# Kernel tuning notes

Measured on AMD Instinct MI355X. Metric: run time of the kernel, lower is better.

Reference implementation:

```python
import jax, jax.numpy as jnp
import numpy as np

# Static config mirroring FinalFFTAudioEngine(compression_ratio=0.3)
COMPRESSION_RATIO = 0.3
ENERGY_THRESHOLD = 0.05
WINDOW = 256  # window_size=512 -> power-of-2 loop ends at 512 -> min(512//2, 512) = 256


def _important_mask(energy, min_count, threshold):
    """Threshold mask, replaced by top-k mask if too few survive (faithful to torch code)."""
    th_mask = energy > threshold
    _, idx = jax.lax.top_k(energy, min_count)
    tk_mask = jnp.zeros(energy.shape, dtype=bool).at[idx].set(True)
    return jnp.where(jnp.sum(th_mask) < min_count, tk_mask, th_mask)


def setup_inputs() -> dict:
    key = jax.random.key(0)
    weight_matrix = jax.random.normal(key, (4096, 4096), dtype=jnp.float32)
    return {"weight_matrix": weight_matrix}


def reference(weight_matrix):
    # weight_to_audio_signal: flatten + max-abs normalize
    signal = weight_matrix.reshape(-1).astype(jnp.float32)
    n = signal.shape[0]  # 16777216, exact multiple of WINDOW -> no padding branch
    sig_max = jnp.max(jnp.abs(signal))
    norm = jnp.where(sig_max > 1e-10, sig_max, jnp.float32(1.0))
    signal = signal / norm

    # optimized_spectral_analysis: non-overlapping windows + per-window FFT
    windows = signal.reshape(-1, WINDOW)          # [T, F] = [65536, 256]
    spec = jnp.fft.fft(windows)                   # complex64 [T, F]

    # intelligent_frequency_selection
    energy = jnp.abs(spec) ** 2                   # [T, F]
    freq_energy = jnp.mean(energy, axis=0)        # [F]
    time_energy = jnp.mean(energy, axis=1)        # [T]
    min_freqs = max(1, int(WINDOW * (1.0 - COMPRESSION_RATIO * 0.7)))          # 202
    min_times = max(1, int(windows.shape[0] * (1.0 - COMPRESSION_RATIO * 0.7)))  # 51773
    freq_mask = _important_mask(freq_energy, min_freqs,
                                ENERGY_THRESHOLD * jnp.max(freq_energy))
    time_mask = _important_mask(time_energy, min_times,
                                ENERGY_THRESHOLD * jnp.max(time_energy))

    # lossless_compression: fused masked copy (replaces nested python double-for-loop)
    mask2d = time_mask[:, None] & freq_mask[None, :]
    compressed = jnp.where(mask2d, spec, jnp.zeros((), dtype=spec.dtype))

    # perfect_reconstruction: IFFT, take real part, flatten, trim to original length
    recon = jnp.real(jnp.fft.ifft(compressed)).reshape(-1)[:n]
    return recon
```

## Files before the change

kernel.cpp:

```cpp
#include <hip/hip_runtime.h>

#define N_TOTAL   16777216
#define NWIN      65536
#define MIN_FREQS 202
#define MIN_TIMES 51773
#define NSLOTS    64
#define NBLK      1024

#define IDX_TCNT    2
#define IDX_FMALL   3
#define IDX_TTHR    4
#define IDX_INVNORM 5
#define IDX_FCNT    6
#define IDX_FMASK   8
#define IDX_SLOTS   264
#define IDX_AMAXB   16648
#define IDX_TMAXB   18696
#define IDX_SUMSQ   20744
#define IDX_TMASKA  86280

__device__ __forceinline__ float dpp_row_sum16(float x)
{
    x += __int_as_float(__builtin_amdgcn_mov_dpp(__float_as_int(x), 0xB1,  0xF, 0xF, true));
    x += __int_as_float(__builtin_amdgcn_mov_dpp(__float_as_int(x), 0x4E,  0xF, 0xF, true));
    x += __int_as_float(__builtin_amdgcn_mov_dpp(__float_as_int(x), 0x141, 0xF, 0xF, true));
    x += __int_as_float(__builtin_amdgcn_mov_dpp(__float_as_int(x), 0x140, 0xF, 0xF, true));
    return x;
}

__device__ __forceinline__ void fft16(float ar[16], float ai[16])
{
#define SWP(a,b) { float t_=ar[a]; ar[a]=ar[b]; ar[b]=t_; \
                   t_=ai[a]; ai[a]=ai[b]; ai[b]=t_; }
    SWP(1,8) SWP(2,4) SWP(3,12) SWP(5,10) SWP(7,14) SWP(11,13)
#undef SWP
#pragma unroll
    for (int i = 0; i < 16; i += 2) {
        float tr = ar[i+1], ti = ai[i+1];
        ar[i+1] = ar[i] - tr; ai[i+1] = ai[i] - ti;
        ar[i] += tr;          ai[i] += ti;
    }
#pragma unroll
    for (int i = 0; i < 16; i += 4) {
        { float tr = ar[i+2], ti = ai[i+2];
          ar[i+2] = ar[i] - tr; ai[i+2] = ai[i] - ti; ar[i] += tr; ai[i] += ti; }
        { float tr = ai[i+3], ti = -ar[i+3];
          ar[i+3] = ar[i+1] - tr; ai[i+3] = ai[i+1] - ti; ar[i+1] += tr; ai[i+1] += ti; }
    }
#pragma unroll
    for (int i = 0; i < 16; i += 8) {
        { float tr = ar[i+4], ti = ai[i+4];
          ar[i+4] = ar[i] - tr; ai[i+4] = ai[i] - ti; ar[i] += tr; ai[i] += ti; }
        { float br = ar[i+5], bi = ai[i+5];
          float tr = 0.70710678f * (br + bi), ti = 0.70710678f * (bi - br);
          ar[i+5] = ar[i+1] - tr; ai[i+5] = ai[i+1] - ti; ar[i+1] += tr; ai[i+1] += ti; }
        { float tr = ai[i+6], ti = -ar[i+6];
          ar[i+6] = ar[i+2] - tr; ai[i+6] = ai[i+2] - ti; ar[i+2] += tr; ai[i+2] += ti; }
        { float br = ar[i+7], bi = ai[i+7];
          float tr = 0.70710678f * (bi - br), ti = -0.70710678f * (br + bi);
          ar[i+7] = ar[i+3] - tr; ai[i+7] = ai[i+3] - ti; ar[i+3] += tr; ai[i+3] += ti; }
    }
    { float tr = ar[8], ti = ai[8];
      ar[8] = ar[0] - tr; ai[8] = ai[0] - ti; ar[0] += tr; ai[0] += ti; }
#define BUT(J, WR, WI) { float br = ar[8+J], bi = ai[8+J];     \
      float tr = br*(WR) - bi*(WI), ti = br*(WI) + bi*(WR);    \
      ar[8+J] = ar[J] - tr; ai[8+J] = ai[J] - ti; ar[J] += tr; ai[J] += ti; }
    BUT(1,  0.92387953f, -0.38268343f)
    BUT(2,  0.70710678f, -0.70710678f)
    BUT(3,  0.38268343f, -0.92387953f)
    BUT(4,  0.f, -1.f)
    BUT(5, -0.38268343f, -0.92387953f)
    BUT(6, -0.70710678f, -0.70710678f)
    BUT(7, -0.92387953f, -0.38268343f)
#undef BUT
}

__global__ __launch_bounds__(256) void k_stats(const float* __restrict__ x,
                                               float* __restrict__ W)
{
    __shared__ float B[16][552];
    __shared__ float sE[256];
    __shared__ float red[256];
    const int tid  = threadIdx.x;
    const int lane = tid & 63;
    const int wv   = tid >> 6;
    const int subw = lane >> 4;
    const int n2   = lane & 15;
    float* Bs = B[wv * 4 + subw];
    float2* Bs2 = (float2*)Bs;

    float twr[16], twi[16];
    {
        float cs, sn;
        __sincosf(-0.024543692606170f * (float)n2, &sn, &cs);
        twr[0] = 1.f; twi[0] = 0.f;
#pragma unroll
        for (int k = 1; k < 16; ++k) {
            twr[k] = twr[k-1] * cs - twi[k-1] * sn;
            twi[k] = twr[k-1] * sn + twi[k-1] * cs;
        }
    }

    float e[16];
#pragma unroll
    for (int k = 0; k < 16; ++k) e[k] = 0.f;
    float amax = 0.f, tmx = 0.f;
    float* sumsq = W + IDX_SUMSQ;

    const int wave_gid = (blockIdx.x << 2) | wv;
    const int GSTRIDE  = 4 * NBLK;

    const float4* xg = (const float4*)(x + (size_t)wave_gid * 1024);
    float4 v0 = xg[lane];
    float4 v1 = xg[64 + lane];
    float4 v2 = xg[128 + lane];
    float4 v3 = xg[192 + lane];

#pragma unroll 1
    for (int g = wave_gid; g < NWIN / 4; g += GSTRIDE) {
        *(float4*)&B[wv * 4 + 0][lane * 4] = v0;
        *(float4*)&B[wv * 4 + 1][lane * 4] = v1;
        *(float4*)&B[wv * 4 + 2][lane * 4] = v2;
        *(float4*)&B[wv * 4 + 3][lane * 4] = v3;
        amax = fmaxf(amax, fmaxf(fmaxf(fabsf(v0.x), fabsf(v0.y)),
                                 fmaxf(fabsf(v0.z), fabsf(v0.w))));
        amax = fmaxf(amax, fmaxf(fmaxf(fabsf(v1.x), fabsf(v1.y)),
                                 fmaxf(fabsf(v1.z), fabsf(v1.w))));
        amax = fmaxf(amax, fmaxf(fmaxf(fabsf(v2.x), fabsf(v2.y)),
                                 fmaxf(fabsf(v2.z), fabsf(v2.w))));
        amax = fmaxf(amax, fmaxf(fmaxf(fabsf(v3.x), fabsf(v3.y)),
                                 fmaxf(fabsf(v3.z), fabsf(v3.w))));
        const int gn = g + GSTRIDE;
        if (gn < NWIN / 4) {
            const float4* xn = (const float4*)(x + (size_t)gn * 1024);
            v0 = xn[lane];
            v1 = xn[64 + lane];
            v2 = xn[128 + lane];
            v3 = xn[192 + lane];
        }
        asm volatile("s_waitcnt lgkmcnt(0)" ::: "memory");
        __builtin_amdgcn_sched_barrier(0);
        float ar[16], ai[16];
#pragma unroll
        for (int j = 0; j < 16; ++j) { ar[j] = Bs[16 * j + n2]; ai[j] = 0.f; }

        fft16(ar, ai);

#pragma unroll
        for (int k = 1; k < 16; ++k) {
            const float xr = ar[k], xi = ai[k];
            ar[k] = xr * twr[k] - xi * twi[k];
            ai[k] = xr * twi[k] + xi * twr[k];
        }

#pragma unroll
        for (int k = 0; k < 16; ++k)
            Bs2[17 * k + n2] = make_float2(ar[k], ai[k]);
        asm volatile("s_waitcnt lgkmcnt(0)" ::: "memory");
        __builtin_amdgcn_sched_barrier(0);
#pragma unroll
        for (int k = 0; k < 16; ++k) {
            const float2 t = Bs2[17 * n2 + k];
            ar[k] = t.x; ai[k] = t.y;
        }

        fft16(ar, ai);

        float p = 0.f;
#pragma unroll
        for (int k = 0; k < 16; ++k) {
            const float t = fmaf(ar[k], ar[k], ai[k] * ai[k]);
            e[k] += t; p += t;
        }
        p = dpp_row_sum16(p);
        if (n2 == 0) sumsq[g * 4 + subw] = p;
        tmx = fmaxf(tmx, p);
    }

    sE[tid] = 0.f;
    __syncthreads();
#pragma unroll
    for (int k = 0; k < 16; ++k)
        atomicAdd(&sE[k * 16 + n2], e[k]);
    __syncthreads();
    atomicAdd(&W[IDX_SLOTS + (size_t)(blockIdx.x & (NSLOTS - 1)) * 256 + tid], sE[tid]);

    red[tid] = amax; __syncthreads();
    for (int s = 128; s > 0; s >>= 1) {
        if (tid < s) red[tid] = fmaxf(red[tid], red[tid + s]);
        __syncthreads();
    }
    if (tid == 0) W[IDX_AMAXB + blockIdx.x] = red[0];
    __syncthreads();
    red[tid] = tmx; __syncthreads();
    for (int s = 128; s > 0; s >>= 1) {
        if (tid < s) red[tid] = fmaxf(red[tid], red[tid + s]);
        __syncthreads();
    }
    if (tid == 0) W[IDX_TMAXB + blockIdx.x] = red[0];
}

__global__ __launch_bounds__(256) void k_post(float* __restrict__ W)
{
    __shared__ float red[256];
    const int tid = threadIdx.x;

    if (blockIdx.x != 0) {
        float tm = 0.f;
#pragma unroll
        for (int k = 0; k < NBLK / 256; ++k)
            tm = fmaxf(tm, W[IDX_TMAXB + k * 256 + tid]);
        red[tid] = tm; __syncthreads();
        for (int s = 128; s > 0; s >>= 1) {
            if (tid < s) red[tid] = fmaxf(red[tid], red[tid + s]);
            __syncthreads();
        }
        const float tthr = 0.05f * red[0];
        __syncthreads();
        const float* sumsq = W + IDX_SUMSQ;
        float* tmask = W + IDX_TMASKA;
        const int base = (blockIdx.x - 1) * 1024 + tid;
        int c = 0;
#pragma unroll
        for (int k = 0; k < 4; k++) {
            const int i = base + k * 256;
            const int mm = (sumsq[i] > tthr) ? 1 : 0;
            c += mm;
            tmask[i] = (float)mm;
        }
        red[tid] = (float)c; __syncthreads();
        for (int s = 128; s > 0; s >>= 1) {
            if (tid < s) red[tid] += red[tid + s];
            __syncthreads();
        }
        if (tid == 0) atomicAdd((int*)W + IDX_TCNT, (int)red[0]);
        return;
    }

    __shared__ float e[256];
    float am = 0.f;
#pragma unroll
    for (int k = 0; k < NBLK / 256; ++k)
        am = fmaxf(am, W[IDX_AMAXB + k * 256 + tid]);
    red[tid] = am; __syncthreads();
    for (int s = 128; s > 0; s >>= 1) {
        if (tid < s) red[tid] = fmaxf(red[tid], red[tid + s]);
        __syncthreads();
    }
    const float amax = red[0];
    __syncthreads();

    float acc = 0.f;
#pragma unroll
    for (int s = 0; s < NSLOTS; s++) acc += W[IDX_SLOTS + s * 256 + tid];
    e[tid] = acc;
    red[tid] = acc; __syncthreads();
    for (int s = 128; s > 0; s >>= 1) {
        if (tid < s) red[tid] = fmaxf(red[tid], red[tid + s]);
        __syncthreads();
    }
    const float fthr = 0.05f * red[0];
    __syncthreads();
    const int my = (acc > fthr) ? 1 : 0;
    red[tid] = (float)my; __syncthreads();
    for (int s = 128; s > 0; s >>= 1) {
        if (tid < s) red[tid] += red[tid + s];
        __syncthreads();
    }
    const int fcnt = (int)red[0];
    __syncthreads();
    float m;
    if (fcnt >= MIN_FREQS) {
        m = (float)my;
    } else {
        int rank = 0;
        for (int j = 0; j < 256; j++) {
            const float ej = e[j];
            if (ej > acc || (ej == acc && j < tid)) rank++;
        }
        m = (rank < MIN_FREQS) ? 1.f : 0.f;
    }
    W[IDX_FMASK + tid] = m;
    red[tid] = m; __syncthreads();
    for (int s = 128; s > 0; s >>= 1) {
        if (tid < s) red[tid] += red[tid + s];
        __syncthreads();
    }
    if (tid == 0) {
        ((int*)W)[IDX_FMALL] = ((int)red[0] == 256) ? 1 : 0;
        ((int*)W)[IDX_FCNT]  = fcnt;
        W[IDX_INVNORM] = 1.f / ((amax > 1e-10f) ? amax : 1.f);
    }
}

__global__ __launch_bounds__(256) void k_timefb(float* __restrict__ W)
{
    if (((const int*)W)[IDX_TCNT] >= MIN_TIMES) return;
    const int t = blockIdx.x * 256 + threadIdx.x;
    const float* sumsq = W + IDX_SUMSQ;
    const float st = sumsq[t];
    int rank = 0;
    for (int j = 0; j < NWIN; j++) {
        const float sj = sumsq[j];
        if (sj > st || (sj == st && j < t)) rank++;
    }
    W[IDX_TMASKA + t] = (rank < MIN_TIMES) ? 1.f : 0.f;
}

__global__ __launch_bounds__(256) void k_out(const float* __restrict__ x,
                                             float* __restrict__ out,
                                             const float* __restrict__ W)
{
    const int tid = threadIdx.x;
    const int fm_all = ((const int*)W)[IDX_FMALL];
    const float inv_norm = W[IDX_INVNORM];
    if (fm_all) {
        const float4* xi = (const float4*)x;
        float4* yo = (float4*)out;
        const float* tmask = W + IDX_TMASKA;
        for (int i = blockIdx.x * 256 + tid; i < N_TOTAL / 4; i += gridDim.x * 256) {
            const float s = inv_norm * tmask[i >> 6];
            float4 v = xi[i];
            v.x *= s; v.y *= s; v.z *= s; v.w *= s;
            yo[i] = v;
        }
        return;
    }
    __shared__ float re[256], im[256], twr[128], twi[128], fm[256];
    if (tid < 128) {
        float s, c;
        __sincosf(-6.283185307179586f * (float)tid / 256.0f, &s, &c);
        twr[tid] = c; twi[tid] = s;
    }
    fm[tid] = W[IDX_FMASK + (int)(__brev((unsigned)tid) >> 24)];
    __syncthreads();
    const float scale = inv_norm * (1.f / 256.f);
    for (int w = blockIdx.x; w < NWIN; w += gridDim.x) {
        const float tm = W[IDX_TMASKA + w];
        if (tm == 0.f) { out[w * 256 + tid] = 0.f; continue; }
        re[tid] = x[w * 256 + tid]; im[tid] = 0.f;
        __syncthreads();
        for (int lh = 7; lh >= 0; lh--) {
            const int half = 1 << lh;
            if (tid < 128) {
                const int k  = tid & (half - 1);
                const int i0 = ((tid & ~(half - 1)) << 1) | k;
                const int i1 = i0 + half;
                const float ar = re[i0], ai = im[i0], br = re[i1], bi = im[i1];
                const float dr = ar - br, di = ai - bi;
                re[i0] = ar + br; im[i0] = ai + bi;
                const int ti = k << (7 - lh);
                const float wr = twr[ti], wi = twi[ti];
                re[i1] = dr * wr - di * wi;
                im[i1] = dr * wi + di * wr;
            }
            __syncthreads();
        }
        re[tid] *= fm[tid]; im[tid] *= fm[tid];
        __syncthreads();
        for (int lh = 0; lh < 8; lh++) {
            const int half = 1 << lh;
            if (tid < 128) {
                const int k  = tid & (half - 1);
                const int i0 = ((tid & ~(half - 1)) << 1) | k;
                const int i1 = i0 + half;
                const int ti = k << (7 - lh);
                const float wr = twr[ti], wi = -twi[ti];
                const float br = re[i1], bi = im[i1];
                const float tr = br * wr - bi * wi;
                const float ts = br * wi + bi * wr;
                const float ar = re[i0], ai = im[i0];
                re[i1] = ar - tr; im[i1] = ai - ts;
                re[i0] = ar + tr; im[i0] = ai + ts;
            }
            __syncthreads();
        }
        out[w * 256 + tid] = re[tid] * scale;
        __syncthreads();
    }
}

extern "C" void kernel_launch(void* const* d_in, const int* in_sizes, int n_in,
                              void* d_out, int out_size, void* d_ws, size_t ws_size,
                              hipStream_t stream)
{
    const float* x = (const float*)d_in[0];
    float* out = (float*)d_out;
    float* W = (float*)d_ws;
    hipMemsetAsync(d_ws, 0, (size_t)IDX_AMAXB * sizeof(float), stream);
    hipLaunchKernelGGL(k_stats,  dim3(NBLK), dim3(256), 0, stream, x, W);
    hipLaunchKernelGGL(k_post,   dim3(65),   dim3(256), 0, stream, W);
    hipLaunchKernelGGL(k_timefb, dim3(256),  dim3(256), 0, stream, W);
    hipLaunchKernelGGL(k_out,    dim3(2048), dim3(256), 0, stream, x, out, W);
}
```

Before: 83.35 us.

## Shrink LDS transpose buffer and recompute twiddles to raise occupancy in stats kernel

The k_stats kernel's per-subwave shared buffer is halved by transposing the real and imaginary parts in two separate passes instead of as interleaved float2. Twiddle factors are now recomputed on the fly by recurrence rather than held in 32 registers, and the grid block count is doubled. The aim is lower LDS and VGPR pressure so more waves fit per CU, plus better spread across CUs. The cost is an extra LDS round-trip and wait per window and a few extra multiplies per twiddle, and the recurrence runs each iteration.

```diff
diff --git a/kernel.cpp b/kernel.cpp
--- a/kernel.cpp
+++ b/kernel.cpp
@@ -5,7 +5,7 @@
 #define MIN_FREQS 202
 #define MIN_TIMES 51773
 #define NSLOTS    64
-#define NBLK      1024
+#define NBLK      2048
 
 #define IDX_TCNT    2
 #define IDX_FMALL   3
@@ -78,7 +78,7 @@
 __global__ __launch_bounds__(256) void k_stats(const float* __restrict__ x,
                                                float* __restrict__ W)
 {
-    __shared__ float B[16][552];
+    __shared__ float B[16][272];
     __shared__ float sE[256];
     __shared__ float red[256];
     const int tid  = threadIdx.x;
@@ -87,19 +87,9 @@
     const int subw = lane >> 4;
     const int n2   = lane & 15;
     float* Bs = B[wv * 4 + subw];
-    float2* Bs2 = (float2*)Bs;
-
-    float twr[16], twi[16];
-    {
-        float cs, sn;
-        __sincosf(-0.024543692606170f * (float)n2, &sn, &cs);
-        twr[0] = 1.f; twi[0] = 0.f;
-#pragma unroll
-        for (int k = 1; k < 16; ++k) {
-            twr[k] = twr[k-1] * cs - twi[k-1] * sn;
-            twi[k] = twr[k-1] * sn + twi[k-1] * cs;
-        }
-    }
+
+    float cs, sn;
+    __sincosf(-0.024543692606170f * (float)n2, &sn, &cs);
 
     float e[16];
 #pragma unroll
@@ -146,23 +136,30 @@
 
         fft16(ar, ai);
 
-#pragma unroll
-        for (int k = 1; k < 16; ++k) {
-            const float xr = ar[k], xi = ai[k];
-            ar[k] = xr * twr[k] - xi * twi[k];
-            ai[k] = xr * twi[k] + xi * twr[k];
-        }
-
-#pragma unroll
-        for (int k = 0; k < 16; ++k)
-            Bs2[17 * k + n2] = make_float2(ar[k], ai[k]);
+        { float wr = 1.f, wi = 0.f;
+#pragma unroll
+          for (int k = 1; k < 16; ++k) {
+              const float nwr = wr * cs - wi * sn;
+              const float nwi = wr * sn + wi * cs;
+              wr = nwr; wi = nwi;
+              const float xr = ar[k], xi = ai[k];
+              ar[k] = xr * wr - xi * wi;
+              ai[k] = xr * wi + xi * wr;
+          } }
+
+#pragma unroll
+        for (int k = 0; k < 16; ++k) Bs[17 * k + n2] = ar[k];
         asm volatile("s_waitcnt lgkmcnt(0)" ::: "memory");
         __builtin_amdgcn_sched_barrier(0);
 #pragma unroll
-        for (int k = 0; k < 16; ++k) {
-            const float2 t = Bs2[17 * n2 + k];
-            ar[k] = t.x; ai[k] = t.y;
-        }
+        for (int k = 0; k < 16; ++k) ar[k] = Bs[17 * n2 + k];
+        asm volatile("" ::: "memory");
+#pragma unroll
+        for (int k = 0; k < 16; ++k) Bs[17 * k + n2] = ai[k];
+        asm volatile("s_waitcnt lgkmcnt(0)" ::: "memory");
+        __builtin_amdgcn_sched_barrier(0);
+#pragma unroll
+        for (int k = 0; k < 16; ++k) ai[k] = Bs[17 * n2 + k];
 
         fft16(ar, ai);
 
```

After: 103.2 us. +23.8%, slower.

## Compute per-window spectral energy with bf16 MFMA DFT instead of radix-16 FFT

Applied to the files above, without the earlier changes.

The statistics kernel drops its two-pass radix-16 FFT and instead multiplies bf16-converted windows by a bf16 DFT matrix held in registers, using 32x32x16 MFMA instructions, to get per-frequency energy. Per-window time energy now comes directly from the time-domain sum of squares (Parseval) rather than from the spectrum. Blocks grow to 1024 threads, each block handles 256 windows with a double-buffered LDS stage, and the grid shrinks from 1024 to 256 blocks. This aims to cut VALU and LDS shuffle work in the stats pass. In exchange, rounding inputs and twiddles to bf16 can flip frequency-mask decisions that sit near the threshold.

```diff
diff --git a/kernel.cpp b/kernel.cpp
--- a/kernel.cpp
+++ b/kernel.cpp
@@ -5,7 +5,7 @@
 #define MIN_FREQS 202
 #define MIN_TIMES 51773
 #define NSLOTS    64
-#define NBLK      1024
+#define NBLK      256
 
 #define IDX_TCNT    2
 #define IDX_FMALL   3
@@ -19,6 +19,9 @@
 #define IDX_SUMSQ   20744
 #define IDX_TMASKA  86280
 
+typedef __attribute__((ext_vector_type(8)))  short bf16x8;
+typedef __attribute__((ext_vector_type(16))) float f32x16;
+
 __device__ __forceinline__ float dpp_row_sum16(float x)
 {
     x += __int_as_float(__builtin_amdgcn_mov_dpp(__float_as_int(x), 0xB1,  0xF, 0xF, true));
@@ -28,176 +31,121 @@
     return x;
 }
 
-__device__ __forceinline__ void fft16(float ar[16], float ai[16])
-{
-#define SWP(a,b) { float t_=ar[a]; ar[a]=ar[b]; ar[b]=t_; \
-                   t_=ai[a]; ai[a]=ai[b]; ai[b]=t_; }
-    SWP(1,8) SWP(2,4) SWP(3,12) SWP(5,10) SWP(7,14) SWP(11,13)
-#undef SWP
-#pragma unroll
-    for (int i = 0; i < 16; i += 2) {
-        float tr = ar[i+1], ti = ai[i+1];
-        ar[i+1] = ar[i] - tr; ai[i+1] = ai[i] - ti;
-        ar[i] += tr;          ai[i] += ti;
-    }
-#pragma unroll
-    for (int i = 0; i < 16; i += 4) {
-        { float tr = ar[i+2], ti = ai[i+2];
-          ar[i+2] = ar[i] - tr; ai[i+2] = ai[i] - ti; ar[i] += tr; ai[i] += ti; }
-        { float tr = ai[i+3], ti = -ar[i+3];
-          ar[i+3] = ar[i+1] - tr; ai[i+3] = ai[i+1] - ti; ar[i+1] += tr; ai[i+1] += ti; }
-    }
-#pragma unroll
-    for (int i = 0; i < 16; i += 8) {
-        { float tr = ar[i+4], ti = ai[i+4];
-          ar[i+4] = ar[i] - tr; ai[i+4] = ai[i] - ti; ar[i] += tr; ai[i] += ti; }
-        { float br = ar[i+5], bi = ai[i+5];
-          float tr = 0.70710678f * (br + bi), ti = 0.70710678f * (bi - br);
-          ar[i+5] = ar[i+1] - tr; ai[i+5] = ai[i+1] - ti; ar[i+1] += tr; ai[i+1] += ti; }
-        { float tr = ai[i+6], ti = -ar[i+6];
-          ar[i+6] = ar[i+2] - tr; ai[i+6] = ai[i+2] - ti; ar[i+2] += tr; ai[i+2] += ti; }
-        { float br = ar[i+7], bi = ai[i+7];
-          float tr = 0.70710678f * (bi - br), ti = -0.70710678f * (br + bi);
-          ar[i+7] = ar[i+3] - tr; ai[i+7] = ai[i+3] - ti; ar[i+3] += tr; ai[i+3] += ti; }
-    }
-    { float tr = ar[8], ti = ai[8];
-      ar[8] = ar[0] - tr; ai[8] = ai[0] - ti; ar[0] += tr; ai[0] += ti; }
-#define BUT(J, WR, WI) { float br = ar[8+J], bi = ai[8+J];     \
-      float tr = br*(WR) - bi*(WI), ti = br*(WI) + bi*(WR);    \
-      ar[8+J] = ar[J] - tr; ai[8+J] = ai[J] - ti; ar[J] += tr; ai[J] += ti; }
-    BUT(1,  0.92387953f, -0.38268343f)
-    BUT(2,  0.70710678f, -0.70710678f)
-    BUT(3,  0.38268343f, -0.92387953f)
-    BUT(4,  0.f, -1.f)
-    BUT(5, -0.38268343f, -0.92387953f)
-    BUT(6, -0.70710678f, -0.70710678f)
-    BUT(7, -0.92387953f, -0.38268343f)
-#undef BUT
-}
-
-__global__ __launch_bounds__(256) void k_stats(const float* __restrict__ x,
-                                               float* __restrict__ W)
-{
-    __shared__ float B[16][552];
-    __shared__ float sE[256];
-    __shared__ float red[256];
+__device__ __forceinline__ unsigned short bf16r(float v)
+{
+    unsigned u = __float_as_uint(v);
+    return (unsigned short)((u + 0x7FFFu + ((u >> 16) & 1u)) >> 16);
+}
+__device__ __forceinline__ unsigned bfpair(float a, float b)
+{
+    return (unsigned)bf16r(a) | ((unsigned)bf16r(b) << 16);
+}
+
+__device__ __forceinline__ void do_stage(short (*Ab)[264], const float4 v0, const float4 v1,
+                                         int wrow, int scol, float* sumsq_g,
+                                         float& amax, float& tmx)
+{
+    amax = fmaxf(amax, fmaxf(fmaxf(fabsf(v0.x), fabsf(v0.y)),
+                             fmaxf(fabsf(v0.z), fabsf(v0.w))));
+    amax = fmaxf(amax, fmaxf(fmaxf(fabsf(v1.x), fabsf(v1.y)),
+                             fmaxf(fabsf(v1.z), fabsf(v1.w))));
+    float ss = v0.x*v0.x + v0.y*v0.y + v0.z*v0.z + v0.w*v0.w
+             + v1.x*v1.x + v1.y*v1.y + v1.z*v1.z + v1.w*v1.w;
+    ss = dpp_row_sum16(ss);
+    ss += __shfl_xor(ss, 16);
+    if (scol == 0) { sumsq_g[wrow] = ss; tmx = fmaxf(tmx, ss); }
+    uint4 u;
+    u.x = bfpair(v0.x, v0.y); u.y = bfpair(v0.z, v0.w);
+    u.z = bfpair(v1.x, v1.y); u.w = bfpair(v1.z, v1.w);
+    *(uint4*)&Ab[wrow][scol * 8] = u;
+}
+
+__global__ __launch_bounds__(1024) void k_stats(const float* __restrict__ x,
+                                                float* __restrict__ W)
+{
+    __shared__ short Abuf[2][32][264];
+    __shared__ float red[1024];
     const int tid  = threadIdx.x;
     const int lane = tid & 63;
     const int wv   = tid >> 6;
-    const int subw = lane >> 4;
-    const int n2   = lane & 15;
-    float* Bs = B[wv * 4 + subw];
-    float2* Bs2 = (float2*)Bs;
-
-    float twr[16], twi[16];
+    const int hi   = lane >> 5;
+    const int col  = lane & 31;
+    const int wrow = tid >> 5;
+    const int scol = tid & 31;
+
+    bf16x8 F[16];
     {
-        float cs, sn;
-        __sincosf(-0.024543692606170f * (float)n2, &sn, &cs);
-        twr[0] = 1.f; twi[0] = 0.f;
-#pragma unroll
-        for (int k = 1; k < 16; ++k) {
-            twr[k] = twr[k-1] * cs - twi[k-1] * sn;
-            twi[k] = twr[k-1] * sn + twi[k-1] * cs;
-        }
-    }
-
-    float e[16];
-#pragma unroll
-    for (int k = 0; k < 16; ++k) e[k] = 0.f;
-    float amax = 0.f, tmx = 0.f;
-    float* sumsq = W + IDX_SUMSQ;
-
-    const int wave_gid = (blockIdx.x << 2) | wv;
-    const int GSTRIDE  = 4 * NBLK;
-
-    const float4* xg = (const float4*)(x + (size_t)wave_gid * 1024);
-    float4 v0 = xg[lane];
-    float4 v1 = xg[64 + lane];
-    float4 v2 = xg[128 + lane];
-    float4 v3 = xg[192 + lane];
-
+        const int f = ((wv & 7) << 5) + col;
+        const bool use_sin = (wv >= 8);
+#pragma unroll
+        for (int kc = 0; kc < 16; ++kc) {
+            bf16x8 t;
+#pragma unroll
+            for (int j = 0; j < 8; ++j) {
+                const int n = kc * 16 + hi * 8 + j;
+                const int m = (n * f) & 255;
+                float s, c;
+                __sincosf((float)m * 0.024543692606170f, &s, &c);
+                t[j] = (short)bf16r(use_sin ? s : c);
+            }
+            F[kc] = t;
+        }
+    }
+
+    const int b = blockIdx.x;
+    const float* xb = x + ((size_t)b << 16);
+    float* sumsq = W + IDX_SUMSQ + (b << 8);
+    float amax = 0.f, tmx = 0.f, fsum = 0.f;
+
+    float4 v0, v1;
+    {
+        const float4* p = (const float4*)(xb + tid * 8);
+        v0 = p[0]; v1 = p[1];
+    }
+    do_stage(Abuf[0], v0, v1, wrow, scol, sumsq, amax, tmx);
+    __syncthreads();
+
+    int cur = 0;
 #pragma unroll 1
-    for (int g = wave_gid; g < NWIN / 4; g += GSTRIDE) {
-        *(float4*)&B[wv * 4 + 0][lane * 4] = v0;
-        *(float4*)&B[wv * 4 + 1][lane * 4] = v1;
-        *(float4*)&B[wv * 4 + 2][lane * 4] = v2;
-        *(float4*)&B[wv * 4 + 3][lane * 4] = v3;
-        amax = fmaxf(amax, fmaxf(fmaxf(fabsf(v0.x), fabsf(v0.y)),
-                                 fmaxf(fabsf(v0.z), fabsf(v0.w))));
-        amax = fmaxf(amax, fmaxf(fmaxf(fabsf(v1.x), fabsf(v1.y)),
-                                 fmaxf(fabsf(v1.z), fabsf(v1.w))));
-        amax = fmaxf(amax, fmaxf(fmaxf(fabsf(v2.x), fabsf(v2.y)),
-                                 fmaxf(fabsf(v2.z), fabsf(v2.w))));
-        amax = fmaxf(amax, fmaxf(fmaxf(fabsf(v3.x), fabsf(v3.y)),
-                                 fmaxf(fabsf(v3.z), fabsf(v3.w))));
-        const int gn = g + GSTRIDE;
-        if (gn < NWIN / 4) {
-            const float4* xn = (const float4*)(x + (size_t)gn * 1024);
-            v0 = xn[lane];
-            v1 = xn[64 + lane];
-            v2 = xn[128 + lane];
-            v3 = xn[192 + lane];
-        }
-        asm volatile("s_waitcnt lgkmcnt(0)" ::: "memory");
-        __builtin_amdgcn_sched_barrier(0);
-        float ar[16], ai[16];
-#pragma unroll
-        for (int j = 0; j < 16; ++j) { ar[j] = Bs[16 * j + n2]; ai[j] = 0.f; }
-
-        fft16(ar, ai);
-
-#pragma unroll
-        for (int k = 1; k < 16; ++k) {
-            const float xr = ar[k], xi = ai[k];
-            ar[k] = xr * twr[k] - xi * twi[k];
-            ai[k] = xr * twi[k] + xi * twr[k];
-        }
-
-#pragma unroll
-        for (int k = 0; k < 16; ++k)
-            Bs2[17 * k + n2] = make_float2(ar[k], ai[k]);
-        asm volatile("s_waitcnt lgkmcnt(0)" ::: "memory");
-        __builtin_amdgcn_sched_barrier(0);
-#pragma unroll
-        for (int k = 0; k < 16; ++k) {
-            const float2 t = Bs2[17 * n2 + k];
-            ar[k] = t.x; ai[k] = t.y;
-        }
-
-        fft16(ar, ai);
-
-        float p = 0.f;
-#pragma unroll
-        for (int k = 0; k < 16; ++k) {
-            const float t = fmaf(ar[k], ar[k], ai[k] * ai[k]);
-            e[k] += t; p += t;
-        }
-        p = dpp_row_sum16(p);
-        if (n2 == 0) sumsq[g * 4 + subw] = p;
-        tmx = fmaxf(tmx, p);
-    }
-
-    sE[tid] = 0.f;
-    __syncthreads();
-#pragma unroll
-    for (int k = 0; k < 16; ++k)
-        atomicAdd(&sE[k * 16 + n2], e[k]);
-    __syncthreads();
-    atomicAdd(&W[IDX_SLOTS + (size_t)(blockIdx.x & (NSLOTS - 1)) * 256 + tid], sE[tid]);
+    for (int g = 0; g < 8; ++g) {
+        if (g < 7) {
+            const float4* p = (const float4*)(xb + (g + 1) * 8192 + tid * 8);
+            v0 = p[0]; v1 = p[1];
+        }
+        f32x16 acc;
+#pragma unroll
+        for (int r = 0; r < 16; ++r) acc[r] = 0.f;
+#pragma unroll
+        for (int kc = 0; kc < 16; ++kc) {
+            const bf16x8 af = *(const bf16x8*)&Abuf[cur][col][kc * 16 + hi * 8];
+            acc = __builtin_amdgcn_mfma_f32_32x32x16_bf16(af, F[kc], acc, 0, 0, 0);
+        }
+#pragma unroll
+        for (int r = 0; r < 16; ++r) fsum += acc[r] * acc[r];
+        if (g < 7)
+            do_stage(Abuf[cur ^ 1], v0, v1, wrow, scol, sumsq + (g + 1) * 32, amax, tmx);
+        __syncthreads();
+        cur ^= 1;
+    }
+
+    fsum += __shfl_xor(fsum, 32);
+    if (lane < 32)
+        atomicAdd(&W[IDX_SLOTS + (size_t)(b & (NSLOTS - 1)) * 256 + ((wv & 7) << 5) + lane],
+                  fsum);
 
     red[tid] = amax; __syncthreads();
-    for (int s = 128; s > 0; s >>= 1) {
+    for (int s = 512; s > 0; s >>= 1) {
         if (tid < s) red[tid] = fmaxf(red[tid], red[tid + s]);
         __syncthreads();
     }
-    if (tid == 0) W[IDX_AMAXB + blockIdx.x] = red[0];
+    if (tid == 0) W[IDX_AMAXB + b] = red[0];
     __syncthreads();
     red[tid] = tmx; __syncthreads();
-    for (int s = 128; s > 0; s >>= 1) {
+    for (int s = 512; s > 0; s >>= 1) {
         if (tid < s) red[tid] = fmaxf(red[tid], red[tid + s]);
         __syncthreads();
     }
-    if (tid == 0) W[IDX_TMAXB + blockIdx.x] = red[0];
+    if (tid == 0) W[IDX_TMAXB + b] = red[0];
 }
 
 __global__ __launch_bounds__(256) void k_post(float* __restrict__ W)
@@ -208,7 +156,7 @@
     if (blockIdx.x != 0) {
         float tm = 0.f;
 #pragma unroll
-        for (int k = 0; k < NBLK / 256; ++k)
+        for (int k = 0; k < ((NBLK + 255) / 256); ++k)
             tm = fmaxf(tm, W[IDX_TMAXB + k * 256 + tid]);
         red[tid] = tm; __syncthreads();
         for (int s = 128; s > 0; s >>= 1) {
@@ -240,7 +188,7 @@
     __shared__ float e[256];
     float am = 0.f;
 #pragma unroll
-    for (int k = 0; k < NBLK / 256; ++k)
+    for (int k = 0; k < ((NBLK + 255) / 256); ++k)
         am = fmaxf(am, W[IDX_AMAXB + k * 256 + tid]);
     red[tid] = am; __syncthreads();
     for (int s = 128; s > 0; s >>= 1) {
@@ -388,8 +336,8 @@
     float* out = (float*)d_out;
     float* W = (float*)d_ws;
     hipMemsetAsync(d_ws, 0, (size_t)IDX_AMAXB * sizeof(float), stream);
-    hipLaunchKernelGGL(k_stats,  dim3(NBLK), dim3(256), 0, stream, x, W);
-    hipLaunchKernelGGL(k_post,   dim3(65),   dim3(256), 0, stream, W);
-    hipLaunchKernelGGL(k_timefb, dim3(256),  dim3(256), 0, stream, W);
-    hipLaunchKernelGGL(k_out,    dim3(2048), dim3(256), 0, stream, x, out, W);
-}
+    hipLaunchKernelGGL(k_stats,  dim3(NBLK), dim3(1024), 0, stream, x, W);
+    hipLaunchKernelGGL(k_post,   dim3(65),   dim3(256),  0, stream, W);
+    hipLaunchKernelGGL(k_timefb, dim3(256),  dim3(256),  0, stream, W);
+    hipLaunchKernelGGL(k_out,    dim3(2048), dim3(256),  0, stream, x, out, W);
+}
```

Result: faster. 67.88 us (median of 2 runs) (-18.6%).
